# Kernel optimization log

Measured on AMD Instinct MI355X. Metric: run time of the kernel, lower is better.

## Reference

```python
import jax, jax.numpy as jnp
import numpy as np

N = 1_000_000
C = 32
DIMS = (480, 360, 32)  # cylindrical voxel grid (z/rho, phi, height)
EPS = 1e-5


def setup_inputs() -> dict:
    rng = np.random.default_rng(0)
    total = DIMS[0] * DIMS[1] * DIMS[2]
    # unique active voxels, sorted so searchsorted gives row indices directly
    ids = np.sort(rng.choice(total, size=N, replace=False)).astype(np.int64)
    z = ids // (DIMS[1] * DIMS[2])
    rem = ids % (DIMS[1] * DIMS[2])
    y = rem // DIMS[2]
    x = rem % DIMS[2]
    coords = np.stack([z, y, x], axis=1)
    strides = np.array([DIMS[1] * DIMS[2], DIMS[2], 1], dtype=np.int64)

    def nbr(delta):
        out = np.full((3, N), -1, dtype=np.int32)
        for a in range(3):
            tgt = ids + delta * strides[a]
            ok = (coords[:, a] + delta >= 0) & (coords[:, a] + delta < DIMS[a])
            pos = np.searchsorted(ids, tgt)
            pos_c = np.clip(pos, 0, N - 1)
            found = ok & (ids[pos_c] == tgt)
            out[a] = np.where(found, pos_c, -1).astype(np.int32)
        return out

    nbr_prev = nbr(-1)
    nbr_next = nbr(+1)

    key = jax.random.key(0)
    k0, k1, k2 = jax.random.split(key, 3)
    features = jax.random.normal(k0, (N, C), dtype=jnp.float32)
    # W[branch, tap, in, out]; taps ordered (-1, 0, +1) along the branch's axis
    W = jax.random.normal(k1, (3, 3, C, C), dtype=jnp.float32) * (1.0 / np.sqrt(3 * C))
    gamma = jnp.ones((3, C), dtype=jnp.float32)
    beta = jnp.zeros((3, C), dtype=jnp.float32)
    mean = jax.random.normal(k2, (3, C), dtype=jnp.float32) * 0.1
    var = jnp.ones((3, C), dtype=jnp.float32)
    return {
        "features": features,
        "nbr_prev": jnp.asarray(nbr_prev),
        "nbr_next": jnp.asarray(nbr_next),
        "W": W,
        "gamma": gamma,
        "beta": beta,
        "mean": mean,
        "var": var,
    }


def _branch(f, Wb, prev, nxt, g, b, m, v):
    # 3-tap submanifold conv along one axis: gather prev/next active neighbors
    pm = prev >= 0
    nm = nxt >= 0
    fp = jnp.where(pm[:, None], f[jnp.where(pm, prev, 0)], 0.0)
    fn = jnp.where(nm[:, None], f[jnp.where(nm, nxt, 0)], 0.0)
    out = fp @ Wb[0] + f @ Wb[1] + fn @ Wb[2]
    # BatchNorm1d (inference stats) + Sigmoid
    out = (out - m) * (g * jax.lax.rsqrt(v + EPS)) + b
    return jax.nn.sigmoid(out)


def reference(features, nbr_prev, nbr_next, W, gamma, beta, mean, var):
    acc = jnp.zeros_like(features)
    for a in range(3):  # conv3x1x1, conv1x3x1, conv1x1x3
        acc = acc + _branch(features, W[a], nbr_prev[a], nbr_next[a],
                            gamma[a], beta[a], mean[a], var[a])
    return acc * features  # sparse_add then gating with input features
```

## Files before the change

kernel.cpp:

```cpp
#include <hip/hip_runtime.h>
#include <stdint.h>


typedef __attribute__((ext_vector_type(8))) __bf16 bf16x8;
typedef __attribute__((ext_vector_type(8))) unsigned short u16x8;
typedef __attribute__((ext_vector_type(4))) float f32x4;
typedef __attribute__((ext_vector_type(2))) float f32x2;

constexpr int NVOX    = 1000000;
constexpr int NTILES  = NVOX / 16;
constexpr int TPW     = 2;
constexpr int WPB     = 4;
constexpr int NWAVES  = (NTILES + TPW - 1) / TPW;
constexpr int NBLOCKS = (NWAVES + WPB - 1) / WPB;
constexpr float LOG2E = 1.4426950408889634f;

constexpr int WS_WELEMS = 18 * 64 * 8;

__global__ __launch_bounds__(256) void prep_kernel(
    const float* __restrict__ Wt,
    const float* __restrict__ gma, const float* __restrict__ bta,
    const float* __restrict__ mea, const float* __restrict__ var,
    unsigned short* __restrict__ wsW, float* __restrict__ wsA,
    float* __restrict__ wsB)
{
    int tid = blockIdx.x * 256 + threadIdx.x;
    if (tid < WS_WELEMS) {
        int f    = tid >> 9;
        int rem  = tid & 511;
        int lane = rem >> 3;
        int j    = rem & 7;
        int br = f / 6, t = (f >> 1) % 3, h = f & 1;
        int n = lane & 15, quad = lane >> 4;
        float w = Wt[((br * 3 + t) * 32 + quad * 8 + j) * 32 + 2 * n + h];
        union { float f; unsigned u; } c; c.f = w;
        wsW[(f * 64 + lane) * 8 + j] = (unsigned short)((c.u + 0x8000u) >> 16);
    } else if (tid < WS_WELEMS + 96) {
        int i = tid - WS_WELEMS;
        float s = gma[i] * __frsqrt_rn(var[i] + 1e-5f);
        wsA[i] = -s * LOG2E;
        wsB[i] = (mea[i] * s - bta[i]) * LOG2E;
    }
}

__device__ __forceinline__ unsigned pack_bf(float a, float b) {
    union { float f; unsigned u; } ca, cb; ca.f = a; cb.f = b;
    return __builtin_amdgcn_perm(cb.u + 0x8000u, ca.u + 0x8000u, 0x07060302u);
}
__device__ __forceinline__ bf16x8 cvt_frag(f32x4 lo, f32x4 hi) {
    union { unsigned u[4]; bf16x8 v; } r;
    r.u[0] = pack_bf(lo[0], lo[1]); r.u[1] = pack_bf(lo[2], lo[3]);
    r.u[2] = pack_bf(hi[0], hi[1]); r.u[3] = pack_bf(hi[2], hi[3]);
    return r.v;
}

__global__ __launch_bounds__(256) void recon_kernel(
    const float*          __restrict__ feat,
    const int*            __restrict__ nprev,
    const int*            __restrict__ nnext,
    const unsigned short* __restrict__ wsW,
    const float*          __restrict__ wsA,
    const float*          __restrict__ wsB,
    float*                __restrict__ out)
{
    const int lane = threadIdx.x & 63;
    const int n    = lane & 15;
    const int quad = lane >> 4;

    int b   = blockIdx.x;
    int per = NBLOCKS / 8;
    int bs  = (b < per * 8) ? ((b & 7) * per + (b >> 3)) : b;
    int wv  = bs * WPB + (threadIdx.x >> 6);

    const int t0 = wv * TPW;
    if (t0 >= NTILES) return;

    bf16x8 Bf[18];
    #pragma unroll
    for (int f = 0; f < 18; ++f)
        Bf[f] = __builtin_bit_cast(bf16x8, *(const u16x8*)(wsW + (f * 64 + lane) * 8));

    f32x2 A_[3], B_[3];
    #pragma unroll
    for (int br = 0; br < 3; ++br) {
        A_[br] = *(const f32x2*)(wsA + br * 32 + 2 * n);
        B_[br] = *(const f32x2*)(wsB + br * 32 + 2 * n);
    }

    int ip[3], inx[3];
    {
        int row0 = t0 * 16 + n;
        #pragma unroll
        for (int a = 0; a < 3; ++a) {
            ip[a]  = nprev[a * NVOX + row0];
            inx[a] = nnext[a * NVOX + row0];
        }
    }

    #pragma unroll 1
    for (int tt = 0; tt < TPW; ++tt) {
        int tile = t0 + tt;
        if (tile >= NTILES) break;
        int base = tile * 16;
        int row  = base + n;

        const f32x4* ps = (const f32x4*)(feat + row * 32 + quad * 8);
        f32x4 s_lo = ps[0], s_hi = ps[1];
        f32x4 p_lo[3], p_hi[3], n_lo[3], n_hi[3];
        #pragma unroll
        for (int a = 0; a < 3; ++a) {
            p_lo[a] = (f32x4){0.f, 0.f, 0.f, 0.f}; p_hi[a] = p_lo[a];
            n_lo[a] = p_lo[a];                     n_hi[a] = p_lo[a];
            if (ip[a] >= 0) {
                const f32x4* pp = (const f32x4*)(feat + ip[a] * 32 + quad * 8);
                p_lo[a] = pp[0]; p_hi[a] = pp[1];
            }
            if (inx[a] >= 0) {
                const f32x4* pn = (const f32x4*)(feat + inx[a] * 32 + quad * 8);
                n_lo[a] = pn[0]; n_hi[a] = pn[1];
            }
        }

        int ipn[3], inn[3];
        if (tt + 1 < TPW && tile + 1 < NTILES) {
            int nrow = row + 16;
            #pragma unroll
            for (int a = 0; a < 3; ++a) {
                ipn[a] = nprev[a * NVOX + nrow];
                inn[a] = nnext[a * NVOX + nrow];
            }
        } else {
            #pragma unroll
            for (int a = 0; a < 3; ++a) { ipn[a] = -1; inn[a] = -1; }
        }

        bf16x8 Aself = cvt_frag(s_lo, s_hi);
        bf16x8 Ap[3], An[3];
        #pragma unroll
        for (int a = 0; a < 3; ++a) {
            Ap[a] = cvt_frag(p_lo[a], p_hi[a]);
            An[a] = cvt_frag(n_lo[a], n_hi[a]);
        }

        f32x4 acc0 = {0.f, 0.f, 0.f, 0.f}, acc1 = {0.f, 0.f, 0.f, 0.f};
        #pragma unroll
        for (int br = 0; br < 3; ++br) {
            f32x4 c0 = {0.f, 0.f, 0.f, 0.f}, c1 = {0.f, 0.f, 0.f, 0.f};
            c0 = __builtin_amdgcn_mfma_f32_16x16x32_bf16(Ap[br], Bf[br*6 + 0], c0, 0, 0, 0);
            c1 = __builtin_amdgcn_mfma_f32_16x16x32_bf16(Ap[br], Bf[br*6 + 1], c1, 0, 0, 0);
            c0 = __builtin_amdgcn_mfma_f32_16x16x32_bf16(Aself,  Bf[br*6 + 2], c0, 0, 0, 0);
            c1 = __builtin_amdgcn_mfma_f32_16x16x32_bf16(Aself,  Bf[br*6 + 3], c1, 0, 0, 0);
            c0 = __builtin_amdgcn_mfma_f32_16x16x32_bf16(An[br], Bf[br*6 + 4], c0, 0, 0, 0);
            c1 = __builtin_amdgcn_mfma_f32_16x16x32_bf16(An[br], Bf[br*6 + 5], c1, 0, 0, 0);
            float a0 = A_[br][0], b0 = B_[br][0], a1 = A_[br][1], b1 = B_[br][1];
            #pragma unroll
            for (int r = 0; r < 4; ++r) {
                float e0 = __builtin_amdgcn_exp2f(__builtin_fmaf(c0[r], a0, b0));
                float e1 = __builtin_amdgcn_exp2f(__builtin_fmaf(c1[r], a1, b1));
                acc0[r] += __builtin_amdgcn_rcpf(1.0f + e0);
                acc1[r] += __builtin_amdgcn_rcpf(1.0f + e1);
            }
        }

        #pragma unroll
        for (int r = 0; r < 4; ++r) {
            int vrow = base + quad * 4 + r;
            f32x2 fv = *(const f32x2*)(feat + vrow * 32 + 2 * n);
            f32x2 ov = { acc0[r] * fv[0], acc1[r] * fv[1] };
            *(f32x2*)(out + vrow * 32 + 2 * n) = ov;
        }

        #pragma unroll
        for (int a = 0; a < 3; ++a) { ip[a] = ipn[a]; inx[a] = inn[a]; }
    }
}

extern "C" void kernel_launch(void* const* d_in, const int* in_sizes, int n_in,
                              void* d_out, int out_size, void* d_ws, size_t ws_size,
                              hipStream_t stream) {
    const float* feat  = (const float*)d_in[0];
    const int*   nprev = (const int*)d_in[1];
    const int*   nnext = (const int*)d_in[2];
    const float* Wt    = (const float*)d_in[3];
    const float* gma   = (const float*)d_in[4];
    const float* bta   = (const float*)d_in[5];
    const float* mea   = (const float*)d_in[6];
    const float* var   = (const float*)d_in[7];
    float*       o     = (float*)d_out;

    unsigned short* wsW = (unsigned short*)d_ws;
    float*          wsA = (float*)((char*)d_ws + WS_WELEMS * 2);
    float*          wsB = wsA + 96;

    prep_kernel<<<(WS_WELEMS + 96 + 255) / 256, 256, 0, stream>>>(
        Wt, gma, bta, mea, var, wsW, wsA, wsB);
    recon_kernel<<<NBLOCKS, 256, 0, stream>>>(feat, nprev, nnext,
                                              wsW, wsA, wsB, o);
}
```

Measured before the change: 317.0 us.

## Stage weights in LDS, prefetch all neighbor indices, branchless masked gathers

Moves the 18 bf16 weight fragments from per-lane registers into shared memory, loaded once per block and read just before each MFMA, and adds a min-blocks launch bound of 3 to cut register pressure and raise occupancy. Neighbor indices for both tiles are loaded up front. Missing neighbors now gather the self row unconditionally and are zeroed with a bitmask after bf16 conversion, which removes divergent branches so all gathers can be in flight together. The costs are extra LDS reads per MFMA, a block-wide barrier at kernel start, and redundant gathers for missing neighbors.

```diff
diff --git a/kernel.cpp b/kernel.cpp
--- a/kernel.cpp
+++ b/kernel.cpp
@@ -6,6 +6,7 @@
 typedef __attribute__((ext_vector_type(8))) unsigned short u16x8;
 typedef __attribute__((ext_vector_type(4))) float f32x4;
 typedef __attribute__((ext_vector_type(2))) float f32x2;
+typedef __attribute__((ext_vector_type(4))) unsigned u32x4;
 
 constexpr int NVOX    = 1000000;
 constexpr int NTILES  = NVOX / 16;
@@ -47,14 +48,15 @@
     union { float f; unsigned u; } ca, cb; ca.f = a; cb.f = b;
     return __builtin_amdgcn_perm(cb.u + 0x8000u, ca.u + 0x8000u, 0x07060302u);
 }
-__device__ __forceinline__ bf16x8 cvt_frag(f32x4 lo, f32x4 hi) {
+__device__ __forceinline__ bf16x8 cvt_mask(f32x4 lo, f32x4 hi, bool act) {
+    unsigned m = act ? 0xffffffffu : 0u;
     union { unsigned u[4]; bf16x8 v; } r;
-    r.u[0] = pack_bf(lo[0], lo[1]); r.u[1] = pack_bf(lo[2], lo[3]);
-    r.u[2] = pack_bf(hi[0], hi[1]); r.u[3] = pack_bf(hi[2], hi[3]);
+    r.u[0] = pack_bf(lo[0], lo[1]) & m; r.u[1] = pack_bf(lo[2], lo[3]) & m;
+    r.u[2] = pack_bf(hi[0], hi[1]) & m; r.u[3] = pack_bf(hi[2], hi[3]) & m;
     return r.v;
 }
 
-__global__ __launch_bounds__(256) void recon_kernel(
+__global__ __launch_bounds__(256, 3) void recon_kernel(
     const float*          __restrict__ feat,
     const int*            __restrict__ nprev,
     const int*            __restrict__ nnext,
@@ -63,6 +65,19 @@
     const float*          __restrict__ wsB,
     float*                __restrict__ out)
 {
+    __shared__ unsigned short sW[WS_WELEMS];
+
+    {
+        const u32x4* src = (const u32x4*)wsW;
+        u32x4*       dst = (u32x4*)sW;
+        #pragma unroll
+        for (int k = 0; k < 5; ++k) {
+            int i = threadIdx.x + k * 256;
+            if (i < WS_WELEMS / 8) dst[i] = src[i];
+        }
+    }
+    __syncthreads();
+
     const int lane = threadIdx.x & 63;
     const int n    = lane & 15;
     const int quad = lane >> 4;
@@ -74,11 +89,6 @@
 
     const int t0 = wv * TPW;
     if (t0 >= NTILES) return;
-
-    bf16x8 Bf[18];
-    #pragma unroll
-    for (int f = 0; f < 18; ++f)
-        Bf[f] = __builtin_bit_cast(bf16x8, *(const u16x8*)(wsW + (f * 64 + lane) * 8));
 
     f32x2 A_[3], B_[3];
     #pragma unroll
@@ -87,17 +97,26 @@
         B_[br] = *(const f32x2*)(wsB + br * 32 + 2 * n);
     }
 
-    int ip[3], inx[3];
-    {
-        int row0 = t0 * 16 + n;
-        #pragma unroll
-        for (int a = 0; a < 3; ++a) {
-            ip[a]  = nprev[a * NVOX + row0];
-            inx[a] = nnext[a * NVOX + row0];
-        }
-    }
-
-    #pragma unroll 1
+    int ip[TPW][3], inx[TPW][3];
+    #pragma unroll
+    for (int tt = 0; tt < TPW; ++tt) {
+        int tile = t0 + tt;
+        int row  = tile * 16 + n;
+        if (tile < NTILES) {
+            #pragma unroll
+            for (int a = 0; a < 3; ++a) {
+                ip[tt][a]  = nprev[a * NVOX + row];
+                inx[tt][a] = nnext[a * NVOX + row];
+            }
+        } else {
+            #pragma unroll
+            for (int a = 0; a < 3; ++a) { ip[tt][a] = -1; inx[tt][a] = -1; }
+        }
+    }
+
+    const u16x8* sWf = (const u16x8*)sW;
+
+    #pragma unroll
     for (int tt = 0; tt < TPW; ++tt) {
         int tile = t0 + tt;
         if (tile >= NTILES) break;
@@ -109,49 +128,38 @@
         f32x4 p_lo[3], p_hi[3], n_lo[3], n_hi[3];
         #pragma unroll
         for (int a = 0; a < 3; ++a) {
-            p_lo[a] = (f32x4){0.f, 0.f, 0.f, 0.f}; p_hi[a] = p_lo[a];
-            n_lo[a] = p_lo[a];                     n_hi[a] = p_lo[a];
-            if (ip[a] >= 0) {
-                const f32x4* pp = (const f32x4*)(feat + ip[a] * 32 + quad * 8);
-                p_lo[a] = pp[0]; p_hi[a] = pp[1];
-            }
-            if (inx[a] >= 0) {
-                const f32x4* pn = (const f32x4*)(feat + inx[a] * 32 + quad * 8);
-                n_lo[a] = pn[0]; n_hi[a] = pn[1];
-            }
-        }
-
-        int ipn[3], inn[3];
-        if (tt + 1 < TPW && tile + 1 < NTILES) {
-            int nrow = row + 16;
-            #pragma unroll
-            for (int a = 0; a < 3; ++a) {
-                ipn[a] = nprev[a * NVOX + nrow];
-                inn[a] = nnext[a * NVOX + nrow];
-            }
-        } else {
-            #pragma unroll
-            for (int a = 0; a < 3; ++a) { ipn[a] = -1; inn[a] = -1; }
-        }
-
-        bf16x8 Aself = cvt_frag(s_lo, s_hi);
+            int rp = ip[tt][a]  >= 0 ? ip[tt][a]  : row;
+            int rn = inx[tt][a] >= 0 ? inx[tt][a] : row;
+            const f32x4* pp = (const f32x4*)(feat + rp * 32 + quad * 8);
+            const f32x4* pn = (const f32x4*)(feat + rn * 32 + quad * 8);
+            p_lo[a] = pp[0]; p_hi[a] = pp[1];
+            n_lo[a] = pn[0]; n_hi[a] = pn[1];
+        }
+
+        bf16x8 Aself = cvt_mask(s_lo, s_hi, true);
         bf16x8 Ap[3], An[3];
         #pragma unroll
         for (int a = 0; a < 3; ++a) {
-            Ap[a] = cvt_frag(p_lo[a], p_hi[a]);
-            An[a] = cvt_frag(n_lo[a], n_hi[a]);
+            Ap[a] = cvt_mask(p_lo[a], p_hi[a], ip[tt][a]  >= 0);
+            An[a] = cvt_mask(n_lo[a], n_hi[a], inx[tt][a] >= 0);
         }
 
         f32x4 acc0 = {0.f, 0.f, 0.f, 0.f}, acc1 = {0.f, 0.f, 0.f, 0.f};
         #pragma unroll
         for (int br = 0; br < 3; ++br) {
             f32x4 c0 = {0.f, 0.f, 0.f, 0.f}, c1 = {0.f, 0.f, 0.f, 0.f};
-            c0 = __builtin_amdgcn_mfma_f32_16x16x32_bf16(Ap[br], Bf[br*6 + 0], c0, 0, 0, 0);
-            c1 = __builtin_amdgcn_mfma_f32_16x16x32_bf16(Ap[br], Bf[br*6 + 1], c1, 0, 0, 0);
-            c0 = __builtin_amdgcn_mfma_f32_16x16x32_bf16(Aself,  Bf[br*6 + 2], c0, 0, 0, 0);
-            c1 = __builtin_amdgcn_mfma_f32_16x16x32_bf16(Aself,  Bf[br*6 + 3], c1, 0, 0, 0);
-            c0 = __builtin_amdgcn_mfma_f32_16x16x32_bf16(An[br], Bf[br*6 + 4], c0, 0, 0, 0);
-            c1 = __builtin_amdgcn_mfma_f32_16x16x32_bf16(An[br], Bf[br*6 + 5], c1, 0, 0, 0);
+            bf16x8 w0 = __builtin_bit_cast(bf16x8, sWf[(br*6 + 0) * 64 + lane]);
+            bf16x8 w1 = __builtin_bit_cast(bf16x8, sWf[(br*6 + 1) * 64 + lane]);
+            c0 = __builtin_amdgcn_mfma_f32_16x16x32_bf16(Ap[br], w0, c0, 0, 0, 0);
+            c1 = __builtin_amdgcn_mfma_f32_16x16x32_bf16(Ap[br], w1, c1, 0, 0, 0);
+            bf16x8 w2 = __builtin_bit_cast(bf16x8, sWf[(br*6 + 2) * 64 + lane]);
+            bf16x8 w3 = __builtin_bit_cast(bf16x8, sWf[(br*6 + 3) * 64 + lane]);
+            c0 = __builtin_amdgcn_mfma_f32_16x16x32_bf16(Aself,  w2, c0, 0, 0, 0);
+            c1 = __builtin_amdgcn_mfma_f32_16x16x32_bf16(Aself,  w3, c1, 0, 0, 0);
+            bf16x8 w4 = __builtin_bit_cast(bf16x8, sWf[(br*6 + 4) * 64 + lane]);
+            bf16x8 w5 = __builtin_bit_cast(bf16x8, sWf[(br*6 + 5) * 64 + lane]);
+            c0 = __builtin_amdgcn_mfma_f32_16x16x32_bf16(An[br], w4, c0, 0, 0, 0);
+            c1 = __builtin_amdgcn_mfma_f32_16x16x32_bf16(An[br], w5, c1, 0, 0, 0);
             float a0 = A_[br][0], b0 = B_[br][0], a1 = A_[br][1], b1 = B_[br][1];
             #pragma unroll
             for (int r = 0; r < 4; ++r) {
@@ -169,9 +177,6 @@
             f32x2 ov = { acc0[r] * fv[0], acc1[r] * fv[1] };
             *(f32x2*)(out + vrow * 32 + 2 * n) = ov;
         }
-
-        #pragma unroll
-        for (int a = 0; a < 3; ++a) { ip[a] = ipn[a]; inx[a] = inn[a]; }
     }
 }
 
```

After: 321.4 us. Within noise of the previous version (+1.4%).
